# Performance work log

Measured on AMD Instinct MI355X. Metric: run time of the kernel, lower is better.

The kernel has to match this reference:

```python
import jax, jax.numpy as jnp
import numpy as np

N = 32          # LPC order
T = 1048576     # number of frames
EPS = 1e-05


def setup_inputs() -> dict:
    key = jax.random.key(0)
    # Diagonally dominant autocorrelation: r0 = 1, sum_k |r_k| <= 0.9 < r0,
    # so the Toeplitz system is positive definite and E stays > 0.
    lags = jax.random.uniform(key, (1, N, T), minval=-1.0, maxval=1.0) * (0.9 / N)
    r0 = jnp.ones((1, 1, T), dtype=jnp.float32)
    pAC = jnp.concatenate([r0, lags.astype(jnp.float32)], axis=1)  # [1, N+1, T]
    return {"pAC": pAC}


def _levinson(pAC):
    ac = pAC[0]                       # [N+1, T]
    E = ac[0]                         # [T]
    lp = jnp.zeros((N, ac.shape[-1]), dtype=pAC.dtype)  # [N, T]
    for i in range(N):                # unrolled over fixed order N (static)
        if i > 0:
            # sum_j lp[j] * ac[i - j], j = 0..i-1  ->  ac[1:i+1] reversed
            acc = jnp.sum(lp[:i] * ac[1:i + 1][::-1], axis=0)
            ki = (ac[i + 1] + acc) / E
        else:
            ki = ac[1] / E
        c = jnp.clip(1.0 - ki * ki, EPS, None)
        E = E * c
        if i > 0:
            # pTmp[j] = lp[j] - ki * lp[i-1-j], from OLD lp (separate buffer)
            lp = lp.at[:i].set(lp[:i] - ki * lp[:i][::-1])
        lp = lp.at[i].set(-ki)
    return lp[None]                   # [1, N, T]


def reference(pAC):
    return _levinson(pAC)
```

## Files before the change

### kernel.cpp

```cpp
#include <hip/hip_runtime.h>

#define LPC_N 32
#define LPC_EPS 1e-5f

__global__ __launch_bounds__(256, 5) void levinson_kernel(
    const float* __restrict__ pAC,
    float* __restrict__ out,
    int T)
{
    int t = blockIdx.x * blockDim.x + threadIdx.x;
    if (t >= T) return;

    float ac[LPC_N + 1];
#pragma unroll
    for (int i = 0; i <= LPC_N; ++i) {
        ac[i] = pAC[(size_t)i * T + t];
    }

    float lp[LPC_N];
    float E = ac[0];

#pragma unroll
    for (int i = 0; i < LPC_N; ++i) {
        float invE = __builtin_amdgcn_rcpf(E);

        float s0 = ac[i + 1];
        float s1 = 0.0f;
#pragma unroll
        for (int j = 0; j + 1 < i; j += 2) {
            s0 += lp[j]     * ac[i - j];
            s1 += lp[j + 1] * ac[i - j - 1];
        }
        if (i & 1) {
            s0 += lp[i - 1] * ac[1];
        }
        float acc = s0 + s1;

        float ki = acc * invE;
        float c  = fmaxf(1.0f - ki * ki, LPC_EPS);
        E *= c;

#pragma unroll
        for (int j = 0; j < i - 1 - j; ++j) {
            float a = lp[j];
            float b = lp[i - 1 - j];
            lp[j]         = a - ki * b;
            lp[i - 1 - j] = b - ki * a;
        }
        if (i & 1) {
            int m = (i - 1) >> 1;
            lp[m] = lp[m] - ki * lp[m];
        }
        lp[i] = -ki;
    }

#pragma unroll
    for (int i = 0; i < LPC_N; ++i) {
        __builtin_nontemporal_store(lp[i], &out[(size_t)i * T + t]);
    }
}

extern "C" void kernel_launch(void* const* d_in, const int* in_sizes, int n_in,
                              void* d_out, int out_size, void* d_ws, size_t ws_size,
                              hipStream_t stream)
{
    const float* pAC = (const float*)d_in[0];
    float* out = (float*)d_out;
    int T = in_sizes[0] / (LPC_N + 1);

    int block = 256;
    int grid = (T + block - 1) / block;
    levinson_kernel<<<grid, block, 0, stream>>>(pAC, out, T);
}
```

Baseline: 245.5 us.

## Process four frames per thread with double-buffered autocorrelation loads

Each thread now handles four frames spaced T/4 apart. Loads for the next frame are issued into a second register buffer before the current frame's recursion runs, so memory latency can overlap with compute. In exchange, register pressure rises, minimum occupancy drops from 5 to 4 waves per SIMD, and the grid shrinks by four times. Frames are silently dropped when T is not divisible by 4.

```diff
diff --git a/kernel.cpp b/kernel.cpp
--- a/kernel.cpp
+++ b/kernel.cpp
@@ -2,21 +2,21 @@
 
 #define LPC_N 32
 #define LPC_EPS 1e-5f
+#define FRAMES 4
 
-__global__ __launch_bounds__(256, 5) void levinson_kernel(
-    const float* __restrict__ pAC,
-    float* __restrict__ out,
-    int T)
+__device__ __forceinline__ void load_ac(float ac[LPC_N + 1],
+                                        const float* __restrict__ pAC,
+                                        int T, int t)
 {
-    int t = blockIdx.x * blockDim.x + threadIdx.x;
-    if (t >= T) return;
+#pragma unroll
+    for (int k = 0; k <= LPC_N; ++k) {
+        ac[k] = pAC[(size_t)k * T + t];
+    }
+}
 
-    float ac[LPC_N + 1];
-#pragma unroll
-    for (int i = 0; i <= LPC_N; ++i) {
-        ac[i] = pAC[(size_t)i * T + t];
-    }
-
+__device__ __forceinline__ void levinson_compute_store(
+    const float ac[LPC_N + 1], float* __restrict__ out, int T, int t)
+{
     float lp[LPC_N];
     float E = ac[0];
 
@@ -60,6 +60,31 @@
     }
 }
 
+__global__ __launch_bounds__(256, 4) void levinson_kernel(
+    const float* __restrict__ pAC,
+    float* __restrict__ out,
+    int T, int nthreads)
+{
+    int t0 = blockIdx.x * blockDim.x + threadIdx.x;
+    if (t0 >= nthreads) return;
+    const int s = nthreads;
+
+    float acA[LPC_N + 1];
+    float acB[LPC_N + 1];
+
+    load_ac(acA, pAC, T, t0);
+    load_ac(acB, pAC, T, t0 + s);
+    levinson_compute_store(acA, out, T, t0);
+
+    load_ac(acA, pAC, T, t0 + 2 * s);
+    levinson_compute_store(acB, out, T, t0 + s);
+
+    load_ac(acB, pAC, T, t0 + 3 * s);
+    levinson_compute_store(acA, out, T, t0 + 2 * s);
+
+    levinson_compute_store(acB, out, T, t0 + 3 * s);
+}
+
 extern "C" void kernel_launch(void* const* d_in, const int* in_sizes, int n_in,
                               void* d_out, int out_size, void* d_ws, size_t ws_size,
                               hipStream_t stream)
@@ -68,7 +93,8 @@
     float* out = (float*)d_out;
     int T = in_sizes[0] / (LPC_N + 1);
 
+    int nthreads = T / FRAMES;
     int block = 256;
-    int grid = (T + block - 1) / block;
-    levinson_kernel<<<grid, block, 0, stream>>>(pAC, out, T);
+    int grid = (nthreads + block - 1) / block;
+    levinson_kernel<<<grid, block, 0, stream>>>(pAC, out, T, nthreads);
 }
```

Measured after the change: 244.9 us. No clear change (-0.3%).

## Spill upper autocorrelation lags to LDS to raise occupancy

Applied to the files above, without the earlier changes.

Keeps the first 17 autocorrelation lags in registers and stages the remaining 16 lags per wave in LDS, reading them back through an accessor inside the recursion. The occupancy hint in launch bounds is raised from 5 to 7 waves so more waves can hide the memory latency. In exchange the inner dot products now issue LDS loads, which add latency and instruction count on every iteration that touches the upper lags.

```diff
diff --git a/kernel.cpp b/kernel.cpp
--- a/kernel.cpp
+++ b/kernel.cpp
@@ -2,20 +2,42 @@
 
 #define LPC_N 32
 #define LPC_EPS 1e-5f
+#define NREG 17
+#define NLDS (LPC_N + 1 - NREG)
 
-__global__ __launch_bounds__(256, 5) void levinson_kernel(
+__global__ __launch_bounds__(256, 7) void levinson_kernel(
     const float* __restrict__ pAC,
     float* __restrict__ out,
     int T)
 {
-    int t = blockIdx.x * blockDim.x + threadIdx.x;
+    __shared__ float smem[4 * NLDS * 64];
+
+    const int tid  = threadIdx.x;
+    const int lane = tid & 63;
+    const int wv   = tid >> 6;
+    const int t    = blockIdx.x * blockDim.x + tid;
     if (t >= T) return;
 
-    float ac[LPC_N + 1];
+    float* wbuf = smem + wv * (NLDS * 64);
+
+    {
+        float hi[NLDS];
 #pragma unroll
-    for (int i = 0; i <= LPC_N; ++i) {
-        ac[i] = pAC[(size_t)i * T + t];
+        for (int k = 0; k < NLDS; ++k)
+            hi[k] = pAC[(size_t)(NREG + k) * T + t];
+#pragma unroll
+        for (int k = 0; k < NLDS; ++k)
+            wbuf[k * 64 + lane] = hi[k];
     }
+
+    float ac[NREG];
+#pragma unroll
+    for (int k = 0; k < NREG; ++k)
+        ac[k] = pAC[(size_t)k * T + t];
+
+    auto AC = [&](int m) -> float {
+        return (m < NREG) ? ac[m] : wbuf[(m - NREG) * 64 + lane];
+    };
 
     float lp[LPC_N];
     float E = ac[0];
@@ -24,12 +46,12 @@
     for (int i = 0; i < LPC_N; ++i) {
         float invE = __builtin_amdgcn_rcpf(E);
 
-        float s0 = ac[i + 1];
+        float s0 = AC(i + 1);
         float s1 = 0.0f;
 #pragma unroll
         for (int j = 0; j + 1 < i; j += 2) {
-            s0 += lp[j]     * ac[i - j];
-            s1 += lp[j + 1] * ac[i - j - 1];
+            s0 += lp[j]     * AC(i - j);
+            s1 += lp[j + 1] * AC(i - j - 1);
         }
         if (i & 1) {
             s0 += lp[i - 1] * ac[1];
```

Measured after the change: 243.6 us. No clear change (-0.8%).
